# Kernel tuning notes

Measured on AMD Instinct MI355X. Metric: run time of the kernel, lower is better.

The kernel has to match this reference:

```python
import jax, jax.numpy as jnp
import numpy as np

N_SRC = 100000
N_TGT = 100000
E = 600000
IN_SRC = 256
IN_TGT = 256
OUT = 128
LEAKY_SLOPE = 0.2


def setup_inputs() -> dict:
    key = jax.random.key(0)
    k0, k1, k2, k3, k4, k5 = jax.random.split(key, 6)
    src = jax.random.normal(k0, (N_SRC, IN_SRC), dtype=jnp.float32)
    tgt = jax.random.normal(k1, (N_TGT, IN_TGT), dtype=jnp.float32)
    # Linear weights stored as [in, out] so forward is x @ W (same math as torch Linear)
    W_src = jax.random.normal(k2, (IN_SRC, OUT), dtype=jnp.float32) * 0.06
    W_tgt = jax.random.normal(k3, (IN_TGT, OUT), dtype=jnp.float32) * 0.06
    a = jax.random.normal(k4, (2 * OUT, 1), dtype=jnp.float32) * 0.1
    edge_index = jax.random.randint(k5, (2, E), 0, N_SRC, dtype=jnp.int64)
    return {"src": src, "tgt": tgt, "W_src": W_src, "W_tgt": W_tgt, "a": a,
            "edge_index": edge_index}


def reference(src, tgt, W_src, W_tgt, a, edge_index):
    out_dim = W_src.shape[1]
    n_src = src.shape[0]
    h_i = src @ W_src  # [N_src, out]
    h_j = tgt @ W_tgt  # [N_tgt, out]
    src_id = edge_index[0]
    tgt_id = edge_index[1]
    # cat([h_i[s], h_j[t]]) @ a == (h_i @ a[:out])[s] + (h_j @ a[out:])[t]
    score_i = h_i @ a[:out_dim, 0]  # [N_src]
    score_j = h_j @ a[out_dim:, 0]  # [N_tgt]
    e = jax.nn.leaky_relu(score_i[src_id] + score_j[tgt_id],
                          negative_slope=LEAKY_SLOPE)  # [E]
    e = jnp.clip(e, -30.0, 30.0)
    exp_e = jnp.exp(e)
    denom = jax.ops.segment_sum(exp_e, src_id, num_segments=n_src)  # [N_src]
    alpha = exp_e / (denom[src_id] + 1e-8)  # [E]  (dropout: eval mode -> identity)
    msg = h_j[tgt_id] * alpha[:, None]  # [E, out]
    out = jax.ops.segment_sum(msg, src_id, num_segments=n_src)  # [N_src, out]
    return jax.nn.elu(out)  # concat=True branch
```

## Files before the change

### kernel.cpp

```cpp
#include <hip/hip_runtime.h>
#include <hip/hip_bf16.h>
#include <math.h>

#define IN_DIM 256
#define OUT_DIM 128
#define LEAKY 0.2f

typedef __attribute__((ext_vector_type(8))) short bf16x8;
typedef __attribute__((ext_vector_type(4))) float f32x4;

__device__ __forceinline__ unsigned short f2bf(float f) {
    union { float f; unsigned int u; } v; v.f = f;
    unsigned int r = v.u + 0x7FFFu + ((v.u >> 16) & 1u);
    return (unsigned short)(r >> 16);
}
__device__ __forceinline__ float bf2f(unsigned int hi16) {
    union { unsigned int u; float f; } v; v.u = hi16 << 16;
    return v.f;
}

__global__ __launch_bounds__(256) void prep_kernel(
    const float* __restrict__ W_src, const float* __restrict__ W_tgt,
    const float* __restrict__ a, float* __restrict__ wcomb,
    unsigned short* __restrict__ Wswz, int4* __restrict__ counts4, int n4) {
    if (blockIdx.x >= 17) {
        int i = (blockIdx.x - 17) * 256 + threadIdx.x;
        if (i < n4) counts4[i] = make_int4(0, 0, 0, 0);
        return;
    }
    if (blockIdx.x == 16) {
        int i = threadIdx.x;
        float s = 0.f;
        #pragma unroll 4
        for (int k = 0; k < OUT_DIM; ++k) s += W_src[i * OUT_DIM + k] * a[k];
        wcomb[i] = s;
        return;
    }
    int idx = blockIdx.x * 256 + threadIdx.x;
    int l  = idx & 63;
    int fj = (idx >> 6) & 7;
    int kc = idx >> 9;
    int col = fj * 16 + (l & 15);
    int kb  = kc * 32 + (l >> 4) * 8;
    unsigned int u[4];
    #pragma unroll
    for (int p = 0; p < 4; ++p) {
        unsigned short e0 = f2bf(W_tgt[(size_t)(kb + 2 * p + 0) * OUT_DIM + col]);
        unsigned short e1 = f2bf(W_tgt[(size_t)(kb + 2 * p + 1) * OUT_DIM + col]);
        u[p] = (unsigned int)e0 | ((unsigned int)e1 << 16);
    }
    *(uint4*)(Wswz + (size_t)idx * 8) = make_uint4(u[0], u[1], u[2], u[3]);
}

__global__ __launch_bounds__(256) void phase1_kernel(
    const float* __restrict__ A, const unsigned short* __restrict__ Wswz,
    const float* __restrict__ a_hi, unsigned short* __restrict__ Hb,
    float* __restrict__ score_j, int Mt, int G,
    const float* __restrict__ X, const float* __restrict__ w,
    float* __restrict__ score_i, int Ms, int V,
    const int* __restrict__ src_id, int* __restrict__ counts,
    int* __restrict__ rank, int E, int H) {
    int b = blockIdx.x;
    int g = b / 9;
    int r = b - g * 9;
    int tid = threadIdx.x;

    if (r == 2 || r == 6 || r == 8) {
        int hb = g * 3 + (r == 6 ? 1 : (r == 8 ? 2 : 0));
        if (hb >= H) return;
        int e = hb * 256 + tid;
        if (e < E) rank[e] = atomicAdd(&counts[src_id[e]], 1);
        return;
    }
    if (r != 0 && r != 4) {
        int vb = g * 4 + (r == 3 ? 1 : (r == 5 ? 2 : (r == 7 ? 3 : 0)));
        if (vb >= V) return;
        int row = vb * 32 + (tid >> 3);
        if (row >= Ms) return;
        int k = tid & 7;
        const float4* R = (const float4*)(X + (size_t)row * IN_DIM);
        const float4* W4 = (const float4*)w;
        float s = 0.f;
        #pragma unroll
        for (int c = 0; c < 8; ++c) {
            float4 x = R[k + 8 * c];
            float4 wv = W4[k + 8 * c];
            s += x.x * wv.x + x.y * wv.y + x.z * wv.z + x.w * wv.w;
        }
        s += __shfl_xor(s, 1);
        s += __shfl_xor(s, 2);
        s += __shfl_xor(s, 4);
        if (k == 0) score_i[row] = s;
        return;
    }
    int gb = g * 2 + (r == 4 ? 1 : 0);
    if (gb >= G) return;
    int w4 = tid >> 6;
    int l = tid & 63;
    int bm = gb * 64;

    int arow = bm + w4 * 16 + (l & 15);
    const float* ap = A + (size_t)(arow < Mt ? arow : Mt - 1) * IN_DIM + (l >> 4) * 8;
    const bf16x8* Wf = (const bf16x8*)Wswz;

    float aw[8];
    #pragma unroll
    for (int j = 0; j < 8; ++j) aw[j] = a_hi[j * 16 + (l & 15)];

    f32x4 acc[8];
    f32x4 zero = {0.f, 0.f, 0.f, 0.f};
    #pragma unroll
    for (int j = 0; j < 8; ++j) acc[j] = zero;

    float4 preA[16];
    #pragma unroll
    for (int kc = 0; kc < 8; ++kc) {
        preA[2 * kc + 0] = *(const float4*)(ap + kc * 32);
        preA[2 * kc + 1] = *(const float4*)(ap + kc * 32 + 4);
    }
    #pragma unroll
    for (int kc = 0; kc < 8; ++kc) {
        float4 a0 = preA[2 * kc + 0];
        float4 a1 = preA[2 * kc + 1];
        union { bf16x8 v; unsigned int u[4]; } fa;
        fa.u[0] = (unsigned int)f2bf(a0.x) | ((unsigned int)f2bf(a0.y) << 16);
        fa.u[1] = (unsigned int)f2bf(a0.z) | ((unsigned int)f2bf(a0.w) << 16);
        fa.u[2] = (unsigned int)f2bf(a1.x) | ((unsigned int)f2bf(a1.y) << 16);
        fa.u[3] = (unsigned int)f2bf(a1.z) | ((unsigned int)f2bf(a1.w) << 16);
        #pragma unroll
        for (int j = 0; j < 8; ++j) {
            bf16x8 bfj = Wf[(size_t)(kc * 8 + j) * 64 + l];
            acc[j] = __builtin_amdgcn_mfma_f32_16x16x32_bf16(fa.v, bfj, acc[j], 0, 0, 0);
        }
    }
    #pragma unroll
    for (int rr = 0; rr < 4; ++rr) {
        int row = bm + w4 * 16 + (l >> 4) * 4 + rr;
        if (row < Mt) {
            float s = 0.f;
            #pragma unroll
            for (int j = 0; j < 8; ++j) {
                float v = acc[j][rr];
                Hb[(size_t)row * OUT_DIM + j * 16 + (l & 15)] = f2bf(v);
                s += v * aw[j];
            }
            s += __shfl_xor(s, 1); s += __shfl_xor(s, 2);
            s += __shfl_xor(s, 4); s += __shfl_xor(s, 8);
            if ((l & 15) == 0) score_j[row] = s;
        }
    }
}

__global__ __launch_bounds__(256) void scan1_kernel(
    const int* __restrict__ counts, int* __restrict__ offs,
    int* __restrict__ blockSums, int n) {
    __shared__ int sd[256];
    int b = blockIdx.x, tid = threadIdx.x;
    int base = b * 1024 + tid * 4;
    int v0 = base + 0 < n ? counts[base + 0] : 0;
    int v1 = base + 1 < n ? counts[base + 1] : 0;
    int v2 = base + 2 < n ? counts[base + 2] : 0;
    int v3 = base + 3 < n ? counts[base + 3] : 0;
    int p1 = v0, p2 = v0 + v1, p3 = v0 + v1 + v2;
    int tsum = p3 + v3;
    sd[tid] = tsum;
    __syncthreads();
    #pragma unroll
    for (int off = 1; off < 256; off <<= 1) {
        int t = tid >= off ? sd[tid - off] : 0;
        __syncthreads();
        sd[tid] += t;
        __syncthreads();
    }
    int ex = sd[tid] - tsum;
    if (base + 0 < n) offs[base + 0] = ex;
    if (base + 1 < n) offs[base + 1] = ex + p1;
    if (base + 2 < n) offs[base + 2] = ex + p2;
    if (base + 3 < n) offs[base + 3] = ex + p3;
    if (tid == 255) blockSums[b] = sd[255];
}

__global__ __launch_bounds__(256) void scan2_kernel(
    const int* __restrict__ blockSums, int* __restrict__ blockOffs, int nb) {
    __shared__ int sd[256];
    int tid = threadIdx.x;
    int v = tid < nb ? blockSums[tid] : 0;
    sd[tid] = v;
    __syncthreads();
    #pragma unroll
    for (int off = 1; off < 256; off <<= 1) {
        int t = tid >= off ? sd[tid - off] : 0;
        __syncthreads();
        sd[tid] += t;
        __syncthreads();
    }
    blockOffs[tid] = sd[tid] - v;
}

__global__ __launch_bounds__(256) void scatter_fused_kernel(
    const int* __restrict__ src_id, const int* __restrict__ tgt_id,
    const float* __restrict__ score_i, const float* __restrict__ score_j,
    const int* __restrict__ offs, const int* __restrict__ blockOffs,
    const int* __restrict__ rank, uint2* __restrict__ pairs, int E) {
    int e = blockIdx.x * blockDim.x + threadIdx.x;
    if (e >= E) return;
    int s = src_id[e], t = tgt_id[e];
    float x = score_i[s] + score_j[t];
    x = x > 0.f ? x : LEAKY * x;
    x = fminf(30.f, fmaxf(-30.f, x));
    float ex = expf(x);
    int p = offs[s] + blockOffs[s >> 10] + rank[e];
    pairs[p] = make_uint2((unsigned int)t, __float_as_uint(ex));
}

__global__ __launch_bounds__(256) void agg_kernel(
    const uint2* __restrict__ pairs, const int* __restrict__ offs,
    const int* __restrict__ blockOffs, const unsigned short* __restrict__ hjb,
    float* __restrict__ out, int N, int E) {
    int node = (int)((blockIdx.x * (long long)blockDim.x + threadIdx.x) >> 6);
    if (node >= N) return;
    int lane = threadIdx.x & 63;
    int q  = lane >> 4;
    int cl = lane & 15;
    int beg = offs[node] + blockOffs[node >> 10];
    int end = (node + 1 < N) ? offs[node + 1] + blockOffs[(node + 1) >> 10] : E;
    int deg = end - beg;
    float den = 0.f;
    float acc[8];
    #pragma unroll
    for (int i = 0; i < 8; ++i) acc[i] = 0.f;

    int iters = (deg + 3) >> 2;
    for (int it = 0; it < iters; ++it) {
        int e = q + 4 * it;
        bool valid = e < deg;
        int idx = beg + (valid ? e : 0);
        uint2 tw = pairs[idx];
        int t = (int)tw.x;
        float wgt = valid ? __uint_as_float(tw.y) : 0.f;
        den += wgt;
        uint4 u = *(const uint4*)(hjb + (size_t)t * OUT_DIM + cl * 8);
        acc[0] += bf2f(u.x & 0xffffu) * wgt;
        acc[1] += bf2f(u.x >> 16) * wgt;
        acc[2] += bf2f(u.y & 0xffffu) * wgt;
        acc[3] += bf2f(u.y >> 16) * wgt;
        acc[4] += bf2f(u.z & 0xffffu) * wgt;
        acc[5] += bf2f(u.z >> 16) * wgt;
        acc[6] += bf2f(u.w & 0xffffu) * wgt;
        acc[7] += bf2f(u.w >> 16) * wgt;
    }
    den += __shfl_xor(den, 16);
    den += __shfl_xor(den, 32);
    float inv = 1.f / (den + 1e-8f);
    #pragma unroll
    for (int i = 0; i < 8; ++i) {
        acc[i] += __shfl_xor(acc[i], 16);
        acc[i] += __shfl_xor(acc[i], 32);
        acc[i] *= inv;
        acc[i] = acc[i] > 0.f ? acc[i] : expm1f(acc[i]);
    }
    if (lane < 16) {
        float4 v0 = make_float4(acc[0], acc[1], acc[2], acc[3]);
        float4 v1 = make_float4(acc[4], acc[5], acc[6], acc[7]);
        *(float4*)(out + (size_t)node * OUT_DIM + cl * 8) = v0;
        *(float4*)(out + (size_t)node * OUT_DIM + cl * 8 + 4) = v1;
    }
}

__global__ __launch_bounds__(256) void edge_pass1_kernel(
    const int* __restrict__ src_id, const int* __restrict__ tgt_id,
    const float* __restrict__ score_i, const float* __restrict__ score_j,
    float* __restrict__ exp_e, float* __restrict__ denom, int E) {
    int e = blockIdx.x * blockDim.x + threadIdx.x;
    if (e >= E) return;
    int s = src_id[e], t = tgt_id[e];
    float x = score_i[s] + score_j[t];
    x = x > 0.f ? x : LEAKY * x;
    x = fminf(30.f, fmaxf(-30.f, x));
    float ex = expf(x);
    exp_e[e] = ex;
    atomicAdd(&denom[s], ex);
}

__global__ __launch_bounds__(256) void edge_pass2_kernel(
    const int* __restrict__ src_id, const int* __restrict__ tgt_id,
    const unsigned short* __restrict__ hjb, const float* __restrict__ exp_e,
    const float* __restrict__ denom, float* __restrict__ out, int E) {
    int idx = blockIdx.x * blockDim.x + threadIdx.x;
    int e = idx >> 6;
    if (e >= E) return;
    int lane = idx & 63;
    int s = src_id[e], t = tgt_id[e];
    float alpha = exp_e[e] / (denom[s] + 1e-8f);
    unsigned int u = *(const unsigned int*)(hjb + (size_t)t * OUT_DIM + lane * 2);
    atomicAdd(out + (size_t)s * OUT_DIM + lane * 2 + 0, bf2f(u & 0xffffu) * alpha);
    atomicAdd(out + (size_t)s * OUT_DIM + lane * 2 + 1, bf2f(u >> 16) * alpha);
}

__global__ __launch_bounds__(256) void elu_kernel(float* __restrict__ out, int n4) {
    int i = blockIdx.x * blockDim.x + threadIdx.x;
    if (i >= n4) return;
    float4 v = ((float4*)out)[i];
    v.x = v.x > 0.f ? v.x : expm1f(v.x);
    v.y = v.y > 0.f ? v.y : expm1f(v.y);
    v.z = v.z > 0.f ? v.z : expm1f(v.z);
    v.w = v.w > 0.f ? v.w : expm1f(v.w);
    ((float4*)out)[i] = v;
}

extern "C" void kernel_launch(void* const* d_in, const int* in_sizes, int n_in,
                              void* d_out, int out_size, void* d_ws, size_t ws_size,
                              hipStream_t stream) {
    const float* src   = (const float*)d_in[0];
    const float* tgt   = (const float*)d_in[1];
    const float* W_src = (const float*)d_in[2];
    const float* W_tgt = (const float*)d_in[3];
    const float* a     = (const float*)d_in[4];
    const int*   edge  = (const int*)d_in[5];

    int N_src = in_sizes[0] / IN_DIM;
    int N_tgt = in_sizes[1] / IN_DIM;
    int E     = in_sizes[5] / 2;
    const int* src_id = edge;
    const int* tgt_id = edge + E;

    float* out = (float*)d_out;

    char* ws = (char*)d_ws;
    size_t off = 0;
    auto alloc = [&](size_t bytes) {
        void* p = ws + off;
        off += (bytes + 255) & ~(size_t)255;
        return p;
    };

    unsigned short* hjb  = (unsigned short*)alloc((size_t)N_tgt * OUT_DIM * 2);
    float* score_i = (float*)alloc((size_t)N_src * 4);
    float* score_j = (float*)alloc((size_t)N_tgt * 4);
    float* wcomb   = (float*)alloc(256 * 4);
    unsigned short* Wswz = (unsigned short*)alloc(4096 * 8 * 2);
    int*   counts    = (int*)alloc(((size_t)N_src + 3) / 4 * 16);
    int*   offs      = (int*)alloc((size_t)(N_src + 1) * 4);
    int*   blockSums = (int*)alloc(256 * 4);
    int*   blockOffs = (int*)alloc(256 * 4);
    float* denom     = (float*)alloc((size_t)N_src * 4);
    float* exp_e     = (float*)alloc((size_t)E * 4);
    size_t fb_need = off;
    int*   rank      = (int*)alloc((size_t)E * 4);
    uint2* pairs     = (uint2*)alloc((size_t)E * 8);
    size_t csr_need = off;
    (void)fb_need;

    bool use_csr = (ws_size >= csr_need);

    int n4 = (N_src + 3) / 4;
    int zblocks = (n4 + 255) / 256;
    prep_kernel<<<17 + zblocks, 256, 0, stream>>>(
        W_src, W_tgt, a, wcomb, Wswz, (int4*)counts, n4);

    int G = (N_tgt + 63) / 64;
    int V = (N_src + 31) / 32;
    int H = (E + 255) / 256;
    int gmax = (G + 1) / 2;
    int vmax = (V + 3) / 4;
    int hmax = (H + 2) / 3;
    int groups = gmax > vmax ? gmax : vmax;
    if (hmax > groups) groups = hmax;
    phase1_kernel<<<groups * 9, 256, 0, stream>>>(
        tgt, Wswz, a + OUT_DIM, hjb, score_j, N_tgt, G,
        src, wcomb, score_i, N_src, V,
        src_id, counts, rank, E, H);

    if (use_csr) {
        int nb = (N_src + 1023) / 1024;
        scan1_kernel<<<nb, 256, 0, stream>>>(counts, offs, blockSums, N_src);
        scan2_kernel<<<1, 256, 0, stream>>>(blockSums, blockOffs, nb);
        scatter_fused_kernel<<<(E + 255) / 256, 256, 0, stream>>>(
            src_id, tgt_id, score_i, score_j, offs, blockOffs, rank, pairs, E);
        agg_kernel<<<(N_src + 3) / 4, 256, 0, stream>>>(
            pairs, offs, blockOffs, hjb, out, N_src, E);
    } else {
        hipMemsetAsync(out, 0, (size_t)N_src * OUT_DIM * sizeof(float), stream);
        hipMemsetAsync(denom, 0, (size_t)N_src * sizeof(float), stream);
        edge_pass1_kernel<<<(E + 255) / 256, 256, 0, stream>>>(
            src_id, tgt_id, score_i, score_j, exp_e, denom, E);
        edge_pass2_kernel<<<(int)(((long long)E * 64 + 255) / 256), 256, 0, stream>>>(
            src_id, tgt_id, hjb, exp_e, denom, out, E);
        elu_kernel<<<(N_src * OUT_DIM / 4 + 255) / 256, 256, 0, stream>>>(
            out, N_src * OUT_DIM / 4);
    }
}
```

Measured before the change: 152.1 us.

## Switch phase1 GEMM to 32x32x16 MFMA with 128-row blocks

Replaces the 16x16x32 bf16 MFMA tiling with 32x32x16 MFMA. Each wave now computes 32 rows by 128 columns, and each GEMM block covers 128 rows instead of 64. The swizzled weight layout in prep_kernel and the epilogue row mapping are rebuilt to match. The block interleave in phase1 goes from 9 slots to 8, so one GEMM block sits per group beside four score-vector blocks and three rank blocks. The A-operand prefetch into registers is dropped in favour of loads inside the loop. The aim is fewer MFMA instructions and less weight-fragment traffic per output, at the risk of higher register pressure, exposed load latency, and a less balanced mix of block types.

After: 327.2 us. 2.15x slower.

```diff
diff --git a/kernel.cpp b/kernel.cpp
--- a/kernel.cpp
+++ b/kernel.cpp
@@ -8,6 +8,7 @@
 
 typedef __attribute__((ext_vector_type(8))) short bf16x8;
 typedef __attribute__((ext_vector_type(4))) float f32x4;
+typedef __attribute__((ext_vector_type(16))) float f32x16;
 
 __device__ __forceinline__ unsigned short f2bf(float f) {
     union { float f; unsigned int u; } v; v.f = f;
@@ -38,10 +39,11 @@
     }
     int idx = blockIdx.x * 256 + threadIdx.x;
     int l  = idx & 63;
-    int fj = (idx >> 6) & 7;
-    int kc = idx >> 9;
-    int col = fj * 16 + (l & 15);
-    int kb  = kc * 32 + (l >> 4) * 8;
+    int f  = idx >> 6;
+    int nc = f & 3;
+    int kc = f >> 2;
+    int col = nc * 32 + (l & 31);
+    int kb  = kc * 16 + (l >> 5) * 8;
     unsigned int u[4];
     #pragma unroll
     for (int p = 0; p < 4; ++p) {
@@ -61,19 +63,19 @@
     const int* __restrict__ src_id, int* __restrict__ counts,
     int* __restrict__ rank, int E, int H) {
     int b = blockIdx.x;
-    int g = b / 9;
-    int r = b - g * 9;
+    int g = b >> 3;
+    int r = b & 7;
     int tid = threadIdx.x;
 
-    if (r == 2 || r == 6 || r == 8) {
-        int hb = g * 3 + (r == 6 ? 1 : (r == 8 ? 2 : 0));
+    if (r != 0 && (r & 1) == 0) {
+        int hb = g * 3 + ((r - 2) >> 1);
         if (hb >= H) return;
         int e = hb * 256 + tid;
         if (e < E) rank[e] = atomicAdd(&counts[src_id[e]], 1);
         return;
     }
-    if (r != 0 && r != 4) {
-        int vb = g * 4 + (r == 3 ? 1 : (r == 5 ? 2 : (r == 7 ? 3 : 0)));
+    if (r & 1) {
+        int vb = g * 4 + ((r - 1) >> 1);
         if (vb >= V) return;
         int row = vb * 32 + (tid >> 3);
         if (row >= Ms) return;
@@ -93,61 +95,59 @@
         if (k == 0) score_i[row] = s;
         return;
     }
-    int gb = g * 2 + (r == 4 ? 1 : 0);
-    if (gb >= G) return;
+    if (g >= G) return;
     int w4 = tid >> 6;
     int l = tid & 63;
-    int bm = gb * 64;
-
-    int arow = bm + w4 * 16 + (l & 15);
-    const float* ap = A + (size_t)(arow < Mt ? arow : Mt - 1) * IN_DIM + (l >> 4) * 8;
+    int bm = g * 128 + w4 * 32;
+    int rl = l & 31;
+    int kh = l >> 5;
+
+    int arow = bm + rl;
+    const float* ap = A + (size_t)(arow < Mt ? arow : Mt - 1) * IN_DIM + kh * 8;
     const bf16x8* Wf = (const bf16x8*)Wswz;
 
-    float aw[8];
-    #pragma unroll
-    for (int j = 0; j < 8; ++j) aw[j] = a_hi[j * 16 + (l & 15)];
-
-    f32x4 acc[8];
-    f32x4 zero = {0.f, 0.f, 0.f, 0.f};
-    #pragma unroll
-    for (int j = 0; j < 8; ++j) acc[j] = zero;
-
-    float4 preA[16];
-    #pragma unroll
-    for (int kc = 0; kc < 8; ++kc) {
-        preA[2 * kc + 0] = *(const float4*)(ap + kc * 32);
-        preA[2 * kc + 1] = *(const float4*)(ap + kc * 32 + 4);
-    }
-    #pragma unroll
-    for (int kc = 0; kc < 8; ++kc) {
-        float4 a0 = preA[2 * kc + 0];
-        float4 a1 = preA[2 * kc + 1];
+    float aw[4];
+    #pragma unroll
+    for (int nc = 0; nc < 4; ++nc) aw[nc] = a_hi[nc * 32 + rl];
+
+    f32x16 acc[4];
+    #pragma unroll
+    for (int nc = 0; nc < 4; ++nc)
+        #pragma unroll
+        for (int q = 0; q < 16; ++q) acc[nc][q] = 0.f;
+
+    #pragma unroll
+    for (int kc = 0; kc < 16; ++kc) {
+        float4 a0 = *(const float4*)(ap + kc * 16);
+        float4 a1 = *(const float4*)(ap + kc * 16 + 4);
         union { bf16x8 v; unsigned int u[4]; } fa;
         fa.u[0] = (unsigned int)f2bf(a0.x) | ((unsigned int)f2bf(a0.y) << 16);
         fa.u[1] = (unsigned int)f2bf(a0.z) | ((unsigned int)f2bf(a0.w) << 16);
         fa.u[2] = (unsigned int)f2bf(a1.x) | ((unsigned int)f2bf(a1.y) << 16);
         fa.u[3] = (unsigned int)f2bf(a1.z) | ((unsigned int)f2bf(a1.w) << 16);
         #pragma unroll
-        for (int j = 0; j < 8; ++j) {
-            bf16x8 bfj = Wf[(size_t)(kc * 8 + j) * 64 + l];
-            acc[j] = __builtin_amdgcn_mfma_f32_16x16x32_bf16(fa.v, bfj, acc[j], 0, 0, 0);
+        for (int nc = 0; nc < 4; ++nc) {
+            bf16x8 bfj = Wf[(size_t)(kc * 4 + nc) * 64 + l];
+            acc[nc] = __builtin_amdgcn_mfma_f32_32x32x16_bf16(fa.v, bfj, acc[nc], 0, 0, 0);
         }
     }
     #pragma unroll
-    for (int rr = 0; rr < 4; ++rr) {
-        int row = bm + w4 * 16 + (l >> 4) * 4 + rr;
-        if (row < Mt) {
-            float s = 0.f;
-            #pragma unroll
-            for (int j = 0; j < 8; ++j) {
-                float v = acc[j][rr];
-                Hb[(size_t)row * OUT_DIM + j * 16 + (l & 15)] = f2bf(v);
-                s += v * aw[j];
-            }
-            s += __shfl_xor(s, 1); s += __shfl_xor(s, 2);
-            s += __shfl_xor(s, 4); s += __shfl_xor(s, 8);
-            if ((l & 15) == 0) score_j[row] = s;
+    for (int reg = 0; reg < 16; ++reg) {
+        int row = bm + (reg & 3) + 8 * (reg >> 2) + 4 * kh;
+        bool ok = row < Mt;
+        float sj = 0.f;
+        #pragma unroll
+        for (int nc = 0; nc < 4; ++nc) {
+            float v = acc[nc][reg];
+            if (ok) Hb[(size_t)row * OUT_DIM + nc * 32 + rl] = f2bf(v);
+            sj += v * aw[nc];
         }
+        sj += __shfl_xor(sj, 1);
+        sj += __shfl_xor(sj, 2);
+        sj += __shfl_xor(sj, 4);
+        sj += __shfl_xor(sj, 8);
+        sj += __shfl_xor(sj, 16);
+        if (rl == 0 && ok) score_j[row] = sj;
     }
 }
 
@@ -358,15 +358,14 @@
     prep_kernel<<<17 + zblocks, 256, 0, stream>>>(
         W_src, W_tgt, a, wcomb, Wswz, (int4*)counts, n4);
 
-    int G = (N_tgt + 63) / 64;
+    int G = (N_tgt + 127) / 128;
     int V = (N_src + 31) / 32;
     int H = (E + 255) / 256;
-    int gmax = (G + 1) / 2;
     int vmax = (V + 3) / 4;
     int hmax = (H + 2) / 3;
-    int groups = gmax > vmax ? gmax : vmax;
+    int groups = G > vmax ? G : vmax;
     if (hmax > groups) groups = hmax;
-    phase1_kernel<<<groups * 9, 256, 0, stream>>>(
+    phase1_kernel<<<groups * 8, 256, 0, stream>>>(
         tgt, Wswz, a + OUT_DIM, hjb, score_j, N_tgt, G,
         src, wcomb, score_i, N_src, V,
         src_id, counts, rank, E, H);
```
